# Performance work log

Hardware: AMD Instinct MI355X
Metric: run time of the kernel (lower is better)

Reference implementation:

```python
import jax, jax.numpy as jnp
import numpy as np

N_HEAD = 16
N_EMBD = 1024
TIME_EMBD = 64
EPS = 1e-5

def _ln(x, w, b):
    mu = jnp.mean(x, axis=-1, keepdims=True)
    var = jnp.mean(jnp.square(x - mu), axis=-1, keepdims=True)
    return (x - mu) * jax.lax.rsqrt(var + EPS) * w + b

def _gelu(x):
    return jax.nn.gelu(x, approximate=False)

def setup_inputs() -> dict:
    key = jax.random.key(0)
    ks = jax.random.split(key, 12)
    B, T, D, TE = 2, 2048, N_EMBD, TIME_EMBD
    C = D + TE  # 1088
    s = lambda fan_in: 1.0 / np.sqrt(fan_in)
    return {
        "z": jax.random.normal(ks[0], (B, T, D), jnp.float32),
        "t": jax.random.uniform(ks[1], (B,), jnp.float32),
        # time_mlp: Linear(1, TE) -> GELU -> Linear(TE, TE)
        "w_t1": jax.random.normal(ks[2], (1, TE), jnp.float32) * s(1),
        "b_t1": jnp.zeros((TE,), jnp.float32),
        "w_t2": jax.random.normal(ks[3], (TE, TE), jnp.float32) * s(TE),
        "b_t2": jnp.zeros((TE,), jnp.float32),
        # attention
        "ln_a_w": jnp.ones((C,), jnp.float32),
        "ln_a_b": jnp.zeros((C,), jnp.float32),
        "w_attn": jax.random.normal(ks[4], (C, 3 * D), jnp.float32) * s(C),
        "b_attn": jnp.zeros((3 * D,), jnp.float32),
        "w_proj": jax.random.normal(ks[5], (D, D), jnp.float32) * s(D),
        "b_proj": jnp.zeros((D,), jnp.float32),
        # mlp
        "ln_m_w": jnp.ones((C,), jnp.float32),
        "ln_m_b": jnp.zeros((C,), jnp.float32),
        "w_fc": jax.random.normal(ks[6], (C, 4 * D), jnp.float32) * s(C),
        "b_fc": jnp.zeros((4 * D,), jnp.float32),
        "w_fc2": jax.random.normal(ks[7], (4 * D, D), jnp.float32) * s(4 * D),
        "b_fc2": jnp.zeros((D,), jnp.float32),
    }

def reference(z, t, w_t1, b_t1, w_t2, b_t2, ln_a_w, ln_a_b, w_attn, b_attn,
              w_proj, b_proj, ln_m_w, ln_m_b, w_fc, b_fc, w_fc2, b_fc2):
    B, T, D = z.shape
    H, hd = N_HEAD, N_EMBD // N_HEAD
    # time embedding: [B, TE] broadcast over T
    t_emb = _gelu(t[:, None] @ w_t1 + b_t1) @ w_t2 + b_t2
    t_emb_bt = jnp.broadcast_to(t_emb[:, None, :], (B, T, TIME_EMBD))
    # --- attention with time-conditioned input ---
    zt = jnp.concatenate([z, t_emb_bt], axis=-1)            # [B,T,D+TE]
    x = _ln(zt, ln_a_w, ln_a_b)
    qkv = x @ w_attn + b_attn                               # [B,T,3D]
    q, k, v = jnp.split(qkv, 3, axis=-1)
    q = q.reshape(B, T, H, hd)
    k = k.reshape(B, T, H, hd)
    v = v.reshape(B, T, H, hd)
    att = jnp.einsum('bqhd,bkhd->bhqk', q, k) * (1.0 / np.sqrt(hd))
    mask = jnp.tril(jnp.ones((T, T), bool))
    att = jnp.where(mask, att, -jnp.inf)
    att = jax.nn.softmax(att, axis=-1)
    y = jnp.einsum('bhqk,bkhd->bqhd', att, v).reshape(B, T, D)
    h = y @ w_proj + b_proj                                 # [B,T,D]
    # --- mlp with time-conditioned input ---
    ht = jnp.concatenate([h, t_emb_bt], axis=-1)
    m = _ln(ht, ln_m_w, ln_m_b)
    dz = _gelu(m @ w_fc + b_fc) @ w_fc2 + b_fc2             # [B,T,D]
    return dz
```

## Files before the change

kernel.cpp:

```cpp
#include <hip/hip_runtime.h>
#include <stdint.h>
#include <math.h>

#define T_SEQ 2048
#define NHEAD 16
#define HD 64
#define DMODEL 1024
#define CDIM 1088
#define MROWS 4096

typedef uint16_t u16;
typedef __bf16 b8v __attribute__((ext_vector_type(8)));
typedef float f4v __attribute__((ext_vector_type(4)));

typedef __attribute__((address_space(3))) void lds_void;
typedef const __attribute__((address_space(1))) void glb_void;

#define GLL(g, l) __builtin_amdgcn_global_load_lds((glb_void*)(g), (lds_void*)(l), 16, 0, 0)

__device__ __forceinline__ float b2f(u16 u) {
  union { uint32_t i; float f; } c; c.i = ((uint32_t)u) << 16; return c.f;
}
__device__ __forceinline__ u16 f2b(float f) {
  union { float f; uint32_t i; } c; c.f = f;
  uint32_t x = c.i;
  return (u16)((x + 0x7fffu + ((x >> 16) & 1u)) >> 16);
}
__device__ __forceinline__ uint32_t cvt_pk_bf16(float lo, float hi) {
  uint32_t r;
  asm("v_cvt_pk_bf16_f32 %0, %1, %2" : "=v"(r) : "v"(lo), "v"(hi));
  return r;
}
__device__ __forceinline__ float exp2_hw(float x) {
  return __builtin_amdgcn_exp2f(x);
}
__device__ __forceinline__ float gelu_f(float x) {
  float ax = fabsf(x);
  float xs = ax * 0.70710678118654752f;
  float t = __frcp_rn(1.0f + 0.3275911f * xs);
  float poly = ((((1.061405429f * t - 1.453152027f) * t + 1.421413741f) * t
                 - 0.284496736f) * t + 0.254829592f) * t;
  float e = __expf(-xs * xs);
  float er = 1.0f - poly * e;
  er = copysignf(er, x);
  return 0.5f * x * (1.0f + er);
}

__global__ void time_mlp_kernel(const float* __restrict__ t, const float* __restrict__ w1,
                                const float* __restrict__ b1, const float* __restrict__ w2,
                                const float* __restrict__ b2, float* __restrict__ temb) {
  __shared__ float h1[2][64];
  int tid = threadIdx.x;
  int b = tid >> 6, i = tid & 63;
  float tv = t[b];
  h1[b][i] = gelu_f(tv * w1[i] + b1[i]);
  __syncthreads();
  float acc = b2[i];
  for (int k = 0; k < 64; ++k) acc += h1[b][k] * w2[k * 64 + i];
  temb[b * 64 + i] = acc;
}

__global__ __launch_bounds__(256) void transpose_kernel(const float* __restrict__ src,
                                                        u16* __restrict__ dst,
                                                        int R, int C) {
  __shared__ u16 tile[32][33];
  int tx = threadIdx.x & 31, ty = threadIdx.x >> 5;
  int c0 = blockIdx.x * 32, r0 = blockIdx.y * 32;
#pragma unroll
  for (int i = 0; i < 4; ++i) {
    int r = ty + i * 8;
    tile[r][tx] = f2b(src[(size_t)(r0 + r) * C + c0 + tx]);
  }
  __syncthreads();
#pragma unroll
  for (int i = 0; i < 4; ++i) {
    int c = ty + i * 8;
    dst[(size_t)(c0 + c) * R + r0 + tx] = tile[tx][c];
  }
}

__global__ __launch_bounds__(256) void add4_kernel(const float4* __restrict__ a,
                                                   const float4* __restrict__ b,
                                                   const float4* __restrict__ c,
                                                   const float4* __restrict__ d,
                                                   float4* __restrict__ o, int n4) {
  int i = blockIdx.x * 256 + threadIdx.x;
  if (i < n4) {
    float4 x = a[i], y = b[i], z = c[i], w = d[i];
    o[i] = float4{x.x + y.x + z.x + w.x, x.y + y.y + z.y + w.y,
                  x.z + y.z + z.z + w.z, x.w + y.w + z.w + w.w};
  }
}

__global__ __launch_bounds__(256) void ln_concat_kernel(const float* __restrict__ zf,
                                                        const float* __restrict__ zf2,
                                                        const float* __restrict__ temb,
                                                        const float* __restrict__ w,
                                                        const float* __restrict__ bvec,
                                                        u16* __restrict__ xout,
                                                        int mode) {
  __shared__ float red[4];
  int row = blockIdx.x;
  int b = row / T_SEQ;
  int tid = threadIdx.x;
  float v[5];
  float sum = 0.f;
#pragma unroll
  for (int i = 0; i < 5; ++i) {
    int c = tid + i * 256;
    float val = 0.f;
    if (c < CDIM) {
      if (c < DMODEL) {
        size_t idx = (size_t)row * DMODEL + c;
        if (mode == 1) val = zf[idx];
        else val = zf[idx] + zf2[idx];
      } else {
        val = temb[b * 64 + (c - DMODEL)];
      }
    }
    v[i] = val;
    sum += val;
  }
#pragma unroll
  for (int off = 32; off; off >>= 1) sum += __shfl_xor(sum, off, 64);
  int wv = tid >> 6, ln = tid & 63;
  if (ln == 0) red[wv] = sum;
  __syncthreads();
  float mean = (red[0] + red[1] + red[2] + red[3]) * (1.0f / CDIM);
  __syncthreads();
  float sq = 0.f;
#pragma unroll
  for (int i = 0; i < 5; ++i) {
    int c = tid + i * 256;
    if (c < CDIM) { float d = v[i] - mean; sq += d * d; }
  }
#pragma unroll
  for (int off = 32; off; off >>= 1) sq += __shfl_xor(sq, off, 64);
  if (ln == 0) red[wv] = sq;
  __syncthreads();
  float inv = rsqrtf((red[0] + red[1] + red[2] + red[3]) * (1.0f / CDIM) + 1e-5f);
#pragma unroll
  for (int i = 0; i < 5; ++i) {
    int c = tid + i * 256;
    if (c < CDIM)
      xout[(size_t)row * CDIM + c] = f2b((v[i] - mean) * inv * w[c] + bvec[c]);
  }
}

__global__ __launch_bounds__(512, 2) void gemm256_kernel(
    const u16* __restrict__ A, const u16* __restrict__ Bt,
    const float* __restrict__ bias,
    void* __restrict__ c0, void* __restrict__ c1,
    void* __restrict__ c2, void* __restrict__ c3,
    int M, int N, int K, int k_tiles, int do_gelu, int out_f32) {
  __shared__ u16 As[2][256 * 64];
  __shared__ u16 Bs[2][256 * 64];
  const int tid = threadIdx.x;
  const int wave = tid >> 6, lane = tid & 63;
  const int wr = wave >> 2, wc = wave & 3;
  const int lrow = lane & 15, quad = lane >> 4;

  int nxy = gridDim.x * gridDim.y;
  int bid = blockIdx.y * gridDim.x + blockIdx.x;
  int cpx = nxy >> 3;
  int swz = (bid & 7) * cpx + (bid >> 3);
  int bx = swz % gridDim.x, by = swz / gridDim.x;
  const int m0 = bx * 256, n0 = by * 256;
  const int kz = blockIdx.z;
  const int kb = kz * k_tiles * 64;
  const int NT = k_tiles;

  const int sr = tid >> 3;
  const int sc = ((tid & 7) ^ ((tid >> 3) & 7)) * 8;
  const u16* gA = A + (size_t)(m0 + sr) * K + kb + sc;
  const u16* gB = Bt + (size_t)(n0 + sr) * K + kb + sc;

  f4v acc[8][4] = {};
  b8v bq[2][4];

  auto STAGE_A = [&](int t, int h) {
    const u16* g = gA + (size_t)(h * 128) * K + t * 64;
    u16* l = (u16*)As[t & 1] + h * 8192 + (wave << 9);
    GLL(g, l);
    GLL(g + (size_t)64 * K, l + 4096);
  };
  auto STAGE_B = [&](int t, int h) {
    const u16* g = gB + (size_t)(h * 128) * K + t * 64;
    u16* l = (u16*)Bs[t & 1] + h * 8192 + (wave << 9);
    GLL(g, l);
    GLL(g + (size_t)64 * K, l + 4096);
  };

  STAGE_A(0, 0); STAGE_B(0, 0); STAGE_B(0, 1);
  STAGE_A(0, 1);
  if (NT > 1) { STAGE_A(1, 0); STAGE_B(1, 0); STAGE_B(1, 1); }
  if (NT > 1) asm volatile("s_waitcnt vmcnt(8)" ::: "memory");
  else        asm volatile("s_waitcnt vmcnt(2)" ::: "memory");
  __builtin_amdgcn_s_barrier();

  for (int t = 0; t < NT; ++t) {
    const char* abase = (const char*)As[t & 1];
    const char* bbase = (const char*)Bs[t & 1];
    const int asw = (lrow & 7) << 4;
    b8v af[4];

#pragma unroll
    for (int j = 0; j < 4; ++j)
      af[j] = *(const b8v*)(abase + (j * 32 + wr * 16 + lrow) * 128 + ((quad * 16) ^ asw));
#pragma unroll
    for (int n = 0; n < 4; ++n)
      bq[0][n] = *(const b8v*)(bbase + (wc * 64 + n * 16 + lrow) * 128 + ((quad * 16) ^ asw));
    if (t + 1 < NT) STAGE_A(t + 1, 1);
    __builtin_amdgcn_s_barrier();
    __builtin_amdgcn_s_setprio(1);
#pragma unroll
    for (int j = 0; j < 4; ++j)
#pragma unroll
      for (int n = 0; n < 4; ++n)
        acc[j][n] = __builtin_amdgcn_mfma_f32_16x16x32_bf16(bq[0][n], af[j], acc[j][n], 0, 0, 0);
    __builtin_amdgcn_s_setprio(0);
    __builtin_amdgcn_s_barrier();

#pragma unroll
    for (int j = 0; j < 4; ++j)
      af[j] = *(const b8v*)(abase + (j * 32 + wr * 16 + lrow) * 128 + ((64 + quad * 16) ^ asw));
#pragma unroll
    for (int n = 0; n < 4; ++n)
      bq[1][n] = *(const b8v*)(bbase + (wc * 64 + n * 16 + lrow) * 128 + ((64 + quad * 16) ^ asw));
    __builtin_amdgcn_s_barrier();
    __builtin_amdgcn_s_setprio(1);
#pragma unroll
    for (int j = 0; j < 4; ++j)
#pragma unroll
      for (int n = 0; n < 4; ++n)
        acc[j][n] = __builtin_amdgcn_mfma_f32_16x16x32_bf16(bq[1][n], af[j], acc[j][n], 0, 0, 0);
    __builtin_amdgcn_s_setprio(0);
    if (t + 1 < NT) asm volatile("s_waitcnt vmcnt(8)" ::: "memory");
    else            asm volatile("s_waitcnt vmcnt(0)" ::: "memory");
    __builtin_amdgcn_s_barrier();

#pragma unroll
    for (int j = 0; j < 4; ++j)
      af[j] = *(const b8v*)(abase + (128 + j * 32 + wr * 16 + lrow) * 128 + ((quad * 16) ^ asw));
    if (t + 2 < NT) { STAGE_B(t + 2, 0); STAGE_A(t + 2, 0); }
    __builtin_amdgcn_s_barrier();
    __builtin_amdgcn_s_setprio(1);
#pragma unroll
    for (int j = 0; j < 4; ++j)
#pragma unroll
      for (int n = 0; n < 4; ++n)
        acc[4 + j][n] = __builtin_amdgcn_mfma_f32_16x16x32_bf16(bq[0][n], af[j], acc[4 + j][n], 0, 0, 0);
    __builtin_amdgcn_s_setprio(0);
    __builtin_amdgcn_s_barrier();

#pragma unroll
    for (int j = 0; j < 4; ++j)
      af[j] = *(const b8v*)(abase + (128 + j * 32 + wr * 16 + lrow) * 128 + ((64 + quad * 16) ^ asw));
    if (t + 2 < NT) STAGE_B(t + 2, 1);
    __builtin_amdgcn_s_barrier();
    __builtin_amdgcn_s_setprio(1);
#pragma unroll
    for (int j = 0; j < 4; ++j)
#pragma unroll
      for (int n = 0; n < 4; ++n)
        acc[4 + j][n] = __builtin_amdgcn_mfma_f32_16x16x32_bf16(bq[1][n], af[j], acc[4 + j][n], 0, 0, 0);
    __builtin_amdgcn_s_setprio(0);
    if (t + 1 < NT) {
      if (t + 2 < NT) asm volatile("s_waitcnt vmcnt(8)" ::: "memory");
      else            asm volatile("s_waitcnt vmcnt(2)" ::: "memory");
    }
    __builtin_amdgcn_s_barrier();
  }

  void* Cout = (kz == 0) ? c0 : (kz == 1) ? c1 : (kz == 2) ? c2 : c3;
#pragma unroll
  for (int mh = 0; mh < 2; ++mh)
#pragma unroll
    for (int j = 0; j < 4; ++j) {
      int grow = m0 + mh * 128 + j * 32 + wr * 16 + lrow;
      size_t rb = (size_t)grow * N;
#pragma unroll
      for (int n = 0; n < 4; ++n) {
        int gcol = n0 + wc * 64 + n * 16 + quad * 4;
        float b0 = 0.f, b1 = 0.f, b2 = 0.f, b3 = 0.f;
        if (kz == 0) {
          float4 bv = *(const float4*)(bias + gcol);
          b0 = bv.x; b1 = bv.y; b2 = bv.z; b3 = bv.w;
        }
        f4v a = acc[mh * 4 + j][n];
        float v0 = a[0] + b0, v1 = a[1] + b1, v2 = a[2] + b2, v3 = a[3] + b3;
        if (do_gelu) {
          v0 = gelu_f(v0); v1 = gelu_f(v1); v2 = gelu_f(v2); v3 = gelu_f(v3);
        }
        if (out_f32) {
          *(float4*)((float*)Cout + rb + gcol) = float4{v0, v1, v2, v3};
        } else {
          ushort4 ov;
          ov.x = f2b(v0); ov.y = f2b(v1); ov.z = f2b(v2); ov.w = f2b(v3);
          *(ushort4*)((u16*)Cout + rb + gcol) = ov;
        }
      }
    }
}

__global__ __launch_bounds__(256) void gemm_splitk2_kernel(const u16* __restrict__ A,
                                                           const u16* __restrict__ Bt,
                                                           const float* __restrict__ bias,
                                                           float* __restrict__ C0,
                                                           float* __restrict__ C1,
                                                           int M, int N, int K, int Kc) {
  __shared__ u16 As[2][128 * 32];
  __shared__ u16 Bs[2][128 * 32];
  const int tid = threadIdx.x;
  const int wave = tid >> 6, lane = tid & 63;
  const int wr = wave >> 1, wc = wave & 1;
  const int m0 = blockIdx.x * 128;
  const int n0 = blockIdx.y * 128;
  const int kz = blockIdx.z;
  const int lrow = lane & 15, quad = lane >> 4;
  const int srow = lane >> 2, sseg = lane & 3;

  const u16* gA0 = A  + (size_t)(m0 + wave * 32 + srow) * K + kz * Kc + sseg * 8;
  const u16* gA1 = gA0 + (size_t)16 * K;
  const u16* gB0 = Bt + (size_t)(n0 + wave * 32 + srow) * K + kz * Kc + sseg * 8;
  const u16* gB1 = gB0 + (size_t)16 * K;
  const int la0 = (wave * 32) * 32, la1 = (wave * 32 + 16) * 32;

  f4v acc[4][4] = {};

  GLL(gA0, &As[0][la0]); GLL(gA1, &As[0][la1]);
  GLL(gB0, &Bs[0][la0]); GLL(gB1, &Bs[0][la1]);

  int cur = 0;
  for (int k0 = 0; k0 < Kc; k0 += 32) {
    __syncthreads();
    if (k0 + 32 < Kc) {
      int nxt = cur ^ 1;
      GLL(gA0 + k0 + 32, &As[nxt][la0]); GLL(gA1 + k0 + 32, &As[nxt][la1]);
      GLL(gB0 + k0 + 32, &Bs[nxt][la0]); GLL(gB1 + k0 + 32, &Bs[nxt][la1]);
    }
    b8v af[4], bfr[4];
#pragma unroll
    for (int mi = 0; mi < 4; ++mi)
      af[mi] = *(const b8v*)(&As[cur][(wr * 64 + mi * 16 + lrow) * 32 + quad * 8]);
#pragma unroll
    for (int ni = 0; ni < 4; ++ni)
      bfr[ni] = *(const b8v*)(&Bs[cur][(wc * 64 + ni * 16 + lrow) * 32 + quad * 8]);
#pragma unroll
    for (int mi = 0; mi < 4; ++mi)
#pragma unroll
      for (int ni = 0; ni < 4; ++ni)
        acc[mi][ni] = __builtin_amdgcn_mfma_f32_16x16x32_bf16(bfr[ni], af[mi], acc[mi][ni], 0, 0, 0);
    cur ^= 1;
  }

  float* C = kz ? C1 : C0;
#pragma unroll
  for (int mi = 0; mi < 4; ++mi) {
    int grow = m0 + wr * 64 + mi * 16 + lrow;
    size_t rb = (size_t)grow * N;
#pragma unroll
    for (int ni = 0; ni < 4; ++ni) {
      int gcol = n0 + wc * 64 + ni * 16 + quad * 4;
      float b0 = 0.f, b1 = 0.f, b2 = 0.f, b3 = 0.f;
      if (kz == 0) {
        float4 bv = *(const float4*)(bias + gcol);
        b0 = bv.x; b1 = bv.y; b2 = bv.z; b3 = bv.w;
      }
      *(float4*)(C + rb + gcol) = float4{acc[mi][ni][0] + b0, acc[mi][ni][1] + b1,
                                         acc[mi][ni][2] + b2, acc[mi][ni][3] + b3};
    }
  }
}

__global__ __launch_bounds__(256) void attn_mfma_kernel(const u16* __restrict__ qkv,
                                                        u16* __restrict__ y) {
  __shared__ u16 Ks[2][64 * 72];
  __shared__ u16 Vts[2][64 * 72];
  __shared__ u16 Ps[64 * 72];
  const int bh = blockIdx.x;
  const int b = bh >> 4, h = bh & 15;
  const int qt = 31 - (int)blockIdx.y;
  const int tid = threadIdx.x, w = tid >> 6, lane = tid & 63;
  const int lrow = lane & 15, quad = lane >> 4;
  const int q0 = qt * 64;
  const int qg = q0 + w * 16 + lrow;

  const int kr = tid >> 2, ksg = tid & 3;
  const int pr = tid >> 3, dsg = tid & 7;
  const u16* kbase = qkv + (size_t)(b * T_SEQ + kr) * 3072 + h * 64 + 1024 + ksg * 16;
  const u16* vbase = qkv + (size_t)(b * T_SEQ + 2 * pr) * 3072 + h * 64 + 2048 + dsg * 8;
  const int keyp = (2 * pr) ^ (dsg * 8);
  const int d0 = dsg * 8;

  uint4 krg0, krg1, vrg0, vrg1;
  auto LOADR = [&](int ct) {
    const u16* ksrc = kbase + (size_t)ct * 64 * 3072;
    krg0 = *(const uint4*)(ksrc);
    krg1 = *(const uint4*)(ksrc + 8);
    const u16* vsrc = vbase + (size_t)ct * 64 * 3072;
    vrg0 = *(const uint4*)(vsrc);
    vrg1 = *(const uint4*)(vsrc + 3072);
  };
  auto WRITE = [&](int bi) {
    *(uint4*)(&Ks[bi][kr * 72 + ksg * 16]) = krg0;
    *(uint4*)(&Ks[bi][kr * 72 + ksg * 16 + 8]) = krg1;
    uint32_t aw[4] = {vrg0.x, vrg0.y, vrg0.z, vrg0.w};
    uint32_t bw[4] = {vrg1.x, vrg1.y, vrg1.z, vrg1.w};
#pragma unroll
    for (int m = 0; m < 4; ++m) {
      *(uint32_t*)(&Vts[bi][(d0 + 2 * m) * 72 + keyp]) =
          __builtin_amdgcn_perm(bw[m], aw[m], 0x05040100u);
      *(uint32_t*)(&Vts[bi][(d0 + 2 * m + 1) * 72 + keyp]) =
          __builtin_amdgcn_perm(bw[m], aw[m], 0x07060302u);
    }
  };

  b8v qf[2];
#pragma unroll
  for (int dc = 0; dc < 2; ++dc)
    qf[dc] = *(const b8v*)(qkv + (size_t)(b * T_SEQ + qg) * 3072 + h * 64 + dc * 32 + quad * 8);

  f4v oacc[4] = {};
  float mrun = -__builtin_inff(), lrun = 0.f;
  const float SC = 0.18033688011112042f;

  LOADR(0);
  WRITE(0);
  __syncthreads();

  const int nch = qt + 1;
  for (int ct = 0; ct < nch; ++ct) {
    const int cur = ct & 1;
    if (ct + 1 < nch) LOADR(ct + 1);

    f4v sacc[4] = {};
    __builtin_amdgcn_s_setprio(1);
#pragma unroll
    for (int ks = 0; ks < 4; ++ks)
#pragma unroll
      for (int dc = 0; dc < 2; ++dc) {
        b8v kf = *(const b8v*)(&Ks[cur][(ks * 16 + lrow) * 72 + dc * 32 + quad * 8]);
        sacc[ks] = __builtin_amdgcn_mfma_f32_16x16x32_bf16(kf, qf[dc], sacc[ks], 0, 0, 0);
      }
    __builtin_amdgcn_s_setprio(0);

    if (ct == qt) {
#pragma unroll
      for (int ks = 0; ks < 4; ++ks)
#pragma unroll
        for (int r = 0; r < 4; ++r) {
          int key = ct * 64 + ks * 16 + quad * 4 + r;
          if (key > qg) sacc[ks][r] = -__builtin_inff();
        }
    }

    float rmax = sacc[0][0];
#pragma unroll
    for (int ks = 0; ks < 4; ++ks)
#pragma unroll
      for (int r = 0; r < 4; ++r) rmax = fmaxf(rmax, sacc[ks][r]);
    rmax = fmaxf(rmax, __shfl_xor(rmax, 16, 64));
    rmax = fmaxf(rmax, __shfl_xor(rmax, 32, 64));
    rmax *= SC;
    float mn = fmaxf(mrun, rmax);
    float al = exp2_hw(mrun - mn);
    mrun = mn;
    float psum = 0.f;
#pragma unroll
    for (int ks = 0; ks < 4; ++ks) {
      float p0 = exp2_hw(fmaf(sacc[ks][0], SC, -mn));
      float p1 = exp2_hw(fmaf(sacc[ks][1], SC, -mn));
      float p2 = exp2_hw(fmaf(sacc[ks][2], SC, -mn));
      float p3 = exp2_hw(fmaf(sacc[ks][3], SC, -mn));
      psum += (p0 + p1) + (p2 + p3);
      uint2 pw;
      pw.x = cvt_pk_bf16(p0, p1);
      pw.y = cvt_pk_bf16(p2, p3);
      *(uint2*)(&Ps[(w * 16 + lrow) * 72 + ks * 16 + quad * 4]) = pw;
    }
    psum += __shfl_xor(psum, 16, 64);
    psum += __shfl_xor(psum, 32, 64);
    lrun = lrun * al + psum;
#pragma unroll
    for (int ds = 0; ds < 4; ++ds) oacc[ds] *= al;

    b8v pf[2];
#pragma unroll
    for (int kc = 0; kc < 2; ++kc)
      pf[kc] = *(const b8v*)(&Ps[(w * 16 + lrow) * 72 + kc * 32 + quad * 8]);
    __builtin_amdgcn_s_setprio(1);
#pragma unroll
    for (int ds = 0; ds < 4; ++ds)
#pragma unroll
      for (int kc = 0; kc < 2; ++kc) {
        int d = ds * 16 + lrow;
        int off = (kc * 32 + quad * 8) ^ (((d >> 3) & 7) * 8);
        b8v vfv = *(const b8v*)(&Vts[cur][d * 72 + off]);
        oacc[ds] = __builtin_amdgcn_mfma_f32_16x16x32_bf16(vfv, pf[kc], oacc[ds], 0, 0, 0);
      }
    __builtin_amdgcn_s_setprio(0);

    if (ct + 1 < nch) {
      WRITE((ct + 1) & 1);
      __syncthreads();
    }
  }

  float rinv = 1.0f / lrun;
  u16* yrow = y + (size_t)(b * T_SEQ + qg) * DMODEL + h * 64;
#pragma unroll
  for (int ds = 0; ds < 4; ++ds) {
    uint2 ov;
    ov.x = cvt_pk_bf16(oacc[ds][0] * rinv, oacc[ds][1] * rinv);
    ov.y = cvt_pk_bf16(oacc[ds][2] * rinv, oacc[ds][3] * rinv);
    *(uint2*)(yrow + ds * 16 + quad * 4) = ov;
  }
}

extern "C" void kernel_launch(void* const* d_in, const int* in_sizes, int n_in,
                              void* d_out, int out_size, void* d_ws, size_t ws_size,
                              hipStream_t stream) {
  const float* z      = (const float*)d_in[0];
  const float* t      = (const float*)d_in[1];
  const float* w_t1   = (const float*)d_in[2];
  const float* b_t1   = (const float*)d_in[3];
  const float* w_t2   = (const float*)d_in[4];
  const float* b_t2   = (const float*)d_in[5];
  const float* ln_a_w = (const float*)d_in[6];
  const float* ln_a_b = (const float*)d_in[7];
  const float* w_attn = (const float*)d_in[8];
  const float* b_attn = (const float*)d_in[9];
  const float* w_proj = (const float*)d_in[10];
  const float* b_proj = (const float*)d_in[11];
  const float* ln_m_w = (const float*)d_in[12];
  const float* ln_m_b = (const float*)d_in[13];
  const float* w_fc   = (const float*)d_in[14];
  const float* b_fc   = (const float*)d_in[15];
  const float* w_fc2  = (const float*)d_in[16];
  const float* b_fc2  = (const float*)d_in[17];

  char* ws = (char*)d_ws;
  float* temb  = (float*)ws;
  u16* wT_attn = (u16*)(ws + 1024);
  u16* wT_proj = wT_attn + (size_t)3072 * 1088;
  u16* wT_fc   = wT_proj + (size_t)1024 * 1024;
  u16* wT_fc2  = wT_fc   + (size_t)4096 * 1088;
  u16* xbuf    = wT_fc2  + (size_t)1024 * 4096;
  u16* big     = xbuf    + (size_t)4096 * 1088;
  u16* ybuf    = big     + (size_t)4096 * 4096;
  float* p0    = (float*)(ybuf + (size_t)4096 * 1024);
  float* p1    = p0 + (size_t)4096 * 1024;
  float* p3    = (float*)wT_attn;

  time_mlp_kernel<<<dim3(1), dim3(128), 0, stream>>>(t, w_t1, b_t1, w_t2, b_t2, temb);

  transpose_kernel<<<dim3(3072 / 32, 1088 / 32), dim3(256), 0, stream>>>(w_attn, wT_attn, 1088, 3072);
  transpose_kernel<<<dim3(1024 / 32, 1024 / 32), dim3(256), 0, stream>>>(w_proj, wT_proj, 1024, 1024);
  transpose_kernel<<<dim3(4096 / 32, 1088 / 32), dim3(256), 0, stream>>>(w_fc, wT_fc, 1088, 4096);
  transpose_kernel<<<dim3(1024 / 32, 4096 / 32), dim3(256), 0, stream>>>(w_fc2, wT_fc2, 4096, 1024);

  ln_concat_kernel<<<dim3(MROWS), dim3(256), 0, stream>>>(
      z, (const float*)nullptr, temb, ln_a_w, ln_a_b, xbuf, 1);

  gemm256_kernel<<<dim3(16, 12, 1), dim3(512), 0, stream>>>(
      xbuf, wT_attn, b_attn, big, nullptr, nullptr, nullptr,
      MROWS, 3072, 1088, 17, 0, 0);

  attn_mfma_kernel<<<dim3(32, 32), dim3(256), 0, stream>>>(big, ybuf);

  gemm_splitk2_kernel<<<dim3(MROWS / 128, 1024 / 128, 2), dim3(256), 0, stream>>>(
      ybuf, wT_proj, b_proj, p0, p1, MROWS, 1024, 1024, 512);

  ln_concat_kernel<<<dim3(MROWS), dim3(256), 0, stream>>>(
      p0, p1, temb, ln_m_w, ln_m_b, xbuf, 2);

  gemm256_kernel<<<dim3(16, 16, 1), dim3(512), 0, stream>>>(
      xbuf, wT_fc, b_fc, big, nullptr, nullptr, nullptr,
      MROWS, 4096, 1088, 17, 1, 0);

  gemm256_kernel<<<dim3(16, 4, 4), dim3(512), 0, stream>>>(
      big, wT_fc2, b_fc2, p0, p1, d_out, p3,
      MROWS, 1024, 4096, 16, 0, 1);

  add4_kernel<<<dim3(MROWS * 1024 / 4 / 256), dim3(256), 0, stream>>>(
      (const float4*)p0, (const float4*)p1, (const float4*)d_out, (const float4*)p3,
      (float4*)d_out, MROWS * 1024 / 4);
}
```

Before: 376.3 us.

## Software-pipeline LDS fragment reads one phase ahead of MFMA in GEMM

Restructures the 256x256 GEMM main loop so each phase's LDS fragment reads for the next MFMA block are issued before the current MFMA block runs. Two A and two B register buffers are ping-ponged, and the next tile's first fragments are prefetched at the end of each iteration. Global-to-LDS staging order and the vmcnt wait counts are retuned to match. The goal is to hide LDS read latency behind matrix work, at the cost of more vector registers, which risks occupancy at 2 blocks per CU, and of trickier waitcnt correctness.

Measured after the change: 385.6 us. 1.02x slower.

```diff
diff --git a/kernel.cpp b/kernel.cpp
--- a/kernel.cpp
+++ b/kernel.cpp
@@ -159,6 +159,7 @@
   const int wave = tid >> 6, lane = tid & 63;
   const int wr = wave >> 2, wc = wave & 3;
   const int lrow = lane & 15, quad = lane >> 4;
+  const int asw = (lrow & 7) << 4;
 
   int nxy = gridDim.x * gridDim.y;
   int bid = blockIdx.y * gridDim.x + blockIdx.x;
@@ -176,7 +177,7 @@
   const u16* gB = Bt + (size_t)(n0 + sr) * K + kb + sc;
 
   f4v acc[8][4] = {};
-  b8v bq[2][4];
+  b8v afX[4], afY[4], bq0[4], bq1[4];
 
   auto STAGE_A = [&](int t, int h) {
     const u16* g = gA + (size_t)(h * 128) * K + t * 64;
@@ -190,85 +191,75 @@
     GLL(g, l);
     GLL(g + (size_t)64 * K, l + 4096);
   };
-
-  STAGE_A(0, 0); STAGE_B(0, 0); STAGE_B(0, 1);
-  STAGE_A(0, 1);
+  auto RD_A = [&](b8v* dst, const char* base, int mh, int kk) {
+#pragma unroll
+    for (int j = 0; j < 4; ++j)
+      dst[j] = *(const b8v*)(base + (mh * 128 + j * 32 + wr * 16 + lrow) * 128 +
+                             ((kk * 64 + quad * 16) ^ asw));
+  };
+  auto RD_B = [&](b8v* dst, const char* base, int kk) {
+#pragma unroll
+    for (int n = 0; n < 4; ++n)
+      dst[n] = *(const b8v*)(base + (wc * 64 + n * 16 + lrow) * 128 +
+                             ((kk * 64 + quad * 16) ^ asw));
+  };
+  auto MFMA16 = [&](b8v* bqv, b8v* afv, int base) {
+#pragma unroll
+    for (int j = 0; j < 4; ++j)
+#pragma unroll
+      for (int n = 0; n < 4; ++n)
+        acc[base + j][n] =
+            __builtin_amdgcn_mfma_f32_16x16x32_bf16(bqv[n], afv[j], acc[base + j][n], 0, 0, 0);
+  };
+
+  STAGE_A(0, 0); STAGE_A(0, 1); STAGE_B(0, 0); STAGE_B(0, 1);
   if (NT > 1) { STAGE_A(1, 0); STAGE_B(1, 0); STAGE_B(1, 1); }
-  if (NT > 1) asm volatile("s_waitcnt vmcnt(8)" ::: "memory");
-  else        asm volatile("s_waitcnt vmcnt(2)" ::: "memory");
+  if (NT > 1) asm volatile("s_waitcnt vmcnt(6)" ::: "memory");
+  else        asm volatile("s_waitcnt vmcnt(0)" ::: "memory");
   __builtin_amdgcn_s_barrier();
+  RD_A(afX, (const char*)As[0], 0, 0);
+  RD_B(bq0, (const char*)Bs[0], 0);
 
   for (int t = 0; t < NT; ++t) {
     const char* abase = (const char*)As[t & 1];
     const char* bbase = (const char*)Bs[t & 1];
-    const int asw = (lrow & 7) << 4;
-    b8v af[4];
-
-#pragma unroll
-    for (int j = 0; j < 4; ++j)
-      af[j] = *(const b8v*)(abase + (j * 32 + wr * 16 + lrow) * 128 + ((quad * 16) ^ asw));
-#pragma unroll
-    for (int n = 0; n < 4; ++n)
-      bq[0][n] = *(const b8v*)(bbase + (wc * 64 + n * 16 + lrow) * 128 + ((quad * 16) ^ asw));
+    const char* anext = (const char*)As[(t + 1) & 1];
+    const char* bnext = (const char*)Bs[(t + 1) & 1];
+
+    RD_A(afY, abase, 0, 1);
+    RD_B(bq1, bbase, 1);
     if (t + 1 < NT) STAGE_A(t + 1, 1);
     __builtin_amdgcn_s_barrier();
     __builtin_amdgcn_s_setprio(1);
-#pragma unroll
-    for (int j = 0; j < 4; ++j)
-#pragma unroll
-      for (int n = 0; n < 4; ++n)
-        acc[j][n] = __builtin_amdgcn_mfma_f32_16x16x32_bf16(bq[0][n], af[j], acc[j][n], 0, 0, 0);
-    __builtin_amdgcn_s_setprio(0);
-    __builtin_amdgcn_s_barrier();
-
-#pragma unroll
-    for (int j = 0; j < 4; ++j)
-      af[j] = *(const b8v*)(abase + (j * 32 + wr * 16 + lrow) * 128 + ((64 + quad * 16) ^ asw));
-#pragma unroll
-    for (int n = 0; n < 4; ++n)
-      bq[1][n] = *(const b8v*)(bbase + (wc * 64 + n * 16 + lrow) * 128 + ((64 + quad * 16) ^ asw));
-    __builtin_amdgcn_s_barrier();
-    __builtin_amdgcn_s_setprio(1);
-#pragma unroll
-    for (int j = 0; j < 4; ++j)
-#pragma unroll
-      for (int n = 0; n < 4; ++n)
-        acc[j][n] = __builtin_amdgcn_mfma_f32_16x16x32_bf16(bq[1][n], af[j], acc[j][n], 0, 0, 0);
+    MFMA16(bq0, afX, 0);
     __builtin_amdgcn_s_setprio(0);
     if (t + 1 < NT) asm volatile("s_waitcnt vmcnt(8)" ::: "memory");
     else            asm volatile("s_waitcnt vmcnt(0)" ::: "memory");
     __builtin_amdgcn_s_barrier();
 
-#pragma unroll
-    for (int j = 0; j < 4; ++j)
-      af[j] = *(const b8v*)(abase + (128 + j * 32 + wr * 16 + lrow) * 128 + ((quad * 16) ^ asw));
-    if (t + 2 < NT) { STAGE_B(t + 2, 0); STAGE_A(t + 2, 0); }
+    RD_A(afX, abase, 1, 0);
     __builtin_amdgcn_s_barrier();
     __builtin_amdgcn_s_setprio(1);
-#pragma unroll
-    for (int j = 0; j < 4; ++j)
-#pragma unroll
-      for (int n = 0; n < 4; ++n)
-        acc[4 + j][n] = __builtin_amdgcn_mfma_f32_16x16x32_bf16(bq[0][n], af[j], acc[4 + j][n], 0, 0, 0);
+    MFMA16(bq1, afY, 0);
     __builtin_amdgcn_s_setprio(0);
     __builtin_amdgcn_s_barrier();
 
-#pragma unroll
-    for (int j = 0; j < 4; ++j)
-      af[j] = *(const b8v*)(abase + (128 + j * 32 + wr * 16 + lrow) * 128 + ((64 + quad * 16) ^ asw));
+    RD_A(afY, abase, 1, 1);
+    if (t + 2 < NT) { STAGE_A(t + 2, 0); STAGE_B(t + 2, 0); }
+    __builtin_amdgcn_s_barrier();
+    __builtin_amdgcn_s_setprio(1);
+    MFMA16(bq0, afX, 4);
+    __builtin_amdgcn_s_setprio(0);
+    if (t + 2 < NT)      asm volatile("s_waitcnt vmcnt(6)" ::: "memory");
+    else if (t + 1 < NT) asm volatile("s_waitcnt vmcnt(2)" ::: "memory");
+    __builtin_amdgcn_s_barrier();
+
+    if (t + 1 < NT) { RD_A(afX, anext, 0, 0); RD_B(bq0, bnext, 0); }
     if (t + 2 < NT) STAGE_B(t + 2, 1);
     __builtin_amdgcn_s_barrier();
     __builtin_amdgcn_s_setprio(1);
-#pragma unroll
-    for (int j = 0; j < 4; ++j)
-#pragma unroll
-      for (int n = 0; n < 4; ++n)
-        acc[4 + j][n] = __builtin_amdgcn_mfma_f32_16x16x32_bf16(bq[1][n], af[j], acc[4 + j][n], 0, 0, 0);
+    MFMA16(bq1, afY, 4);
     __builtin_amdgcn_s_setprio(0);
-    if (t + 1 < NT) {
-      if (t + 2 < NT) asm volatile("s_waitcnt vmcnt(8)" ::: "memory");
-      else            asm volatile("s_waitcnt vmcnt(2)" ::: "memory");
-    }
     __builtin_amdgcn_s_barrier();
   }
 
```
